# Kernel tuning notes

Hardware: AMD Instinct MI355X
Metric: run time of the kernel (lower is better)

The kernel has to match this reference:

```python
import jax, jax.numpy as jnp
import numpy as np

MARGIN = 1.0
EPS = 1e-16


def _pairwise_dist(x):
    # Euclidean cdist, p=2: sqrt(||a||^2 + ||b||^2 - 2 a.b), clamped, with
    # a safe sqrt so the (zero-distance) diagonal has zero gradient like torch.cdist.
    sq = jnp.sum(x * x, axis=1)  # [N]
    d2 = sq[:, None] + sq[None, :] - 2.0 * (x @ x.T)  # [N, N]
    d2 = jnp.maximum(d2, 0.0)
    return jnp.where(d2 > 0.0, jnp.sqrt(jnp.where(d2 > 0.0, d2, 1.0)), 0.0)


def setup_inputs() -> dict:
    key = jax.random.key(0)
    k1, k2 = jax.random.split(key)
    embeddings = jax.random.normal(k1, (384, 512), dtype=jnp.float32)
    labels = jax.random.randint(k2, (384,), 0, 24, dtype=jnp.int64)
    return {"embeddings": embeddings, "labels": labels}


def reference(embeddings, labels):
    dist = _pairwise_dist(embeddings)  # [N, N]
    pos = (labels[:, None] == labels[None, :]).astype(embeddings.dtype)  # [N, N]
    neg = 1.0 - pos
    positive_dist = dist * pos
    negative_dist = dist * neg
    # triplet_loss[a, p, n] = d(a,p)*pos - d(a,n)*neg + margin
    triplet_loss = jax.nn.relu(positive_dist[:, :, None] - negative_dist[:, None, :] + MARGIN)
    valid = pos[:, :, None] * neg[:, None, :]  # [N, N, N]
    num_valid = jnp.sum(valid) + EPS
    return jnp.sum(triplet_loss * valid) / num_valid
```

## Files before the change

kernel.cpp:

```cpp
#include <hip/hip_runtime.h>


#define NPTS 384
#define DIM  512
#define TS   32
#define BK   64
#define PITCH 68
#define NT1  256
#define NT2  384
#define NW2  (NT2 / 64)

__global__ __launch_bounds__(NT1) void dist_tile(const float* __restrict__ X,
                                                 float* __restrict__ D) {
    __shared__ float As[TS * PITCH];
    __shared__ float Bs[TS * PITCH];
    const int t  = threadIdx.x;
    const int tx = t & 15, ty = t >> 4;
    const int bi = blockIdx.y * TS;
    const int bj = blockIdx.x * TS;

    const float4* X4 = (const float4*)X;
    const int r0 = t >> 4, c4 = t & 15;

    float4 pa0, pa1, pb0, pb1;
    int k4 = 0;
    {
        pa0 = X4[(size_t)(bi + r0)      * (DIM/4) + k4 + c4];
        pa1 = X4[(size_t)(bi + r0 + 16) * (DIM/4) + k4 + c4];
        pb0 = X4[(size_t)(bj + r0)      * (DIM/4) + k4 + c4];
        pb1 = X4[(size_t)(bj + r0 + 16) * (DIM/4) + k4 + c4];
        *(float4*)&As[ r0       * PITCH + c4*4] = pa0;
        *(float4*)&As[(r0 + 16) * PITCH + c4*4] = pa1;
        *(float4*)&Bs[ r0       * PITCH + c4*4] = pb0;
        *(float4*)&Bs[(r0 + 16) * PITCH + c4*4] = pb1;
    }
    __syncthreads();

    float acc00 = 0.f, acc01 = 0.f, acc10 = 0.f, acc11 = 0.f;

    for (int kt = 0; kt < DIM / BK; ++kt) {
        if (kt < DIM / BK - 1) {
            k4 = (kt + 1) * (BK / 4);
            pa0 = X4[(size_t)(bi + r0)      * (DIM/4) + k4 + c4];
            pa1 = X4[(size_t)(bi + r0 + 16) * (DIM/4) + k4 + c4];
            pb0 = X4[(size_t)(bj + r0)      * (DIM/4) + k4 + c4];
            pb1 = X4[(size_t)(bj + r0 + 16) * (DIM/4) + k4 + c4];
        }
#pragma unroll
        for (int kk = 0; kk < BK / 4; ++kk) {
            const float4 a0 = *(const float4*)&As[(2*ty)   * PITCH + kk*4];
            const float4 a1 = *(const float4*)&As[(2*ty+1) * PITCH + kk*4];
            const float4 b0 = *(const float4*)&Bs[(2*tx)   * PITCH + kk*4];
            const float4 b1 = *(const float4*)&Bs[(2*tx+1) * PITCH + kk*4];
            float d;
            d = a0.x - b0.x; acc00 = fmaf(d, d, acc00);
            d = a0.y - b0.y; acc00 = fmaf(d, d, acc00);
            d = a0.z - b0.z; acc00 = fmaf(d, d, acc00);
            d = a0.w - b0.w; acc00 = fmaf(d, d, acc00);
            d = a0.x - b1.x; acc01 = fmaf(d, d, acc01);
            d = a0.y - b1.y; acc01 = fmaf(d, d, acc01);
            d = a0.z - b1.z; acc01 = fmaf(d, d, acc01);
            d = a0.w - b1.w; acc01 = fmaf(d, d, acc01);
            d = a1.x - b0.x; acc10 = fmaf(d, d, acc10);
            d = a1.y - b0.y; acc10 = fmaf(d, d, acc10);
            d = a1.z - b0.z; acc10 = fmaf(d, d, acc10);
            d = a1.w - b0.w; acc10 = fmaf(d, d, acc10);
            d = a1.x - b1.x; acc11 = fmaf(d, d, acc11);
            d = a1.y - b1.y; acc11 = fmaf(d, d, acc11);
            d = a1.z - b1.z; acc11 = fmaf(d, d, acc11);
            d = a1.w - b1.w; acc11 = fmaf(d, d, acc11);
        }
        __syncthreads();
        if (kt < DIM / BK - 1) {
            *(float4*)&As[ r0       * PITCH + c4*4] = pa0;
            *(float4*)&As[(r0 + 16) * PITCH + c4*4] = pa1;
            *(float4*)&Bs[ r0       * PITCH + c4*4] = pb0;
            *(float4*)&Bs[(r0 + 16) * PITCH + c4*4] = pb1;
            __syncthreads();
        }
    }

    const int gi = bi + 2*ty, gj = bj + 2*tx;
    *(float2*)&D[(size_t)gi      * NPTS + gj] = make_float2(sqrtf(acc00), sqrtf(acc01));
    *(float2*)&D[(size_t)(gi+1)  * NPTS + gj] = make_float2(sqrtf(acc10), sqrtf(acc11));
}

__global__ __launch_bounds__(NT2) void pair_reduce(const float* __restrict__ D,
                                                   const int* __restrict__ labels,
                                                   float* __restrict__ out) {
    __shared__ float s_dp[NPTS];
    __shared__ float s_dn[NPTS];
    __shared__ int   s_lab[NPTS] __attribute__((aligned(16)));
    __shared__ int   s_cp[NW2], s_cn[NW2];
    __shared__ float s_red[NW2];
    __shared__ int   s_nv[NW2];

    const int t = threadIdx.x, lane = t & 63, w = t >> 6;
    const int a = blockIdx.x;

    const float dv = D[(size_t)a * NPTS + t];
    s_lab[t] = labels[t];
    const int lab_a = labels[a];
    __syncthreads();

    const bool isp = (s_lab[t] == lab_a);
    const unsigned long long m = __ballot(isp);
    if (lane == 0) { s_cp[w] = __popcll(m); s_cn[w] = 64 - __popcll(m); }
    __syncthreads();

    int basep = 0, basen = 0, np = 0, nn = 0;
#pragma unroll
    for (int i = 0; i < NW2; ++i) {
        if (i < w) { basep += s_cp[i]; basen += s_cn[i]; }
        np += s_cp[i]; nn += s_cn[i];
    }
    const unsigned long long blw = (1ull << lane) - 1ull;
    if (isp) s_dp[basep + __popcll(m  & blw)] = dv;
    else     s_dn[basen + __popcll(~m & blw)] = dv;
    __syncthreads();

    const bool  va  = (t < nn);
    const float dna = va ? s_dn[t] : 0.f;
    float local = 0.f;
    for (int p = 0; p < np; ++p) {
        const float c = s_dp[p] + 1.0f;
        if (va) local += fmaxf(c - dna, 0.f);
    }

    const int myl = s_lab[t];
    int npt = 0;
    const int4* L4 = (const int4*)s_lab;
#pragma unroll 8
    for (int j4 = 0; j4 < NPTS / 4; ++j4) {
        const int4 l = L4[j4];
        npt += (l.x == myl) + (l.y == myl) + (l.z == myl) + (l.w == myl);
    }
    int nvl = npt * (NPTS - npt);

    for (int off = 32; off; off >>= 1) {
        local += __shfl_down(local, off, 64);
        nvl   += __shfl_down(nvl,   off, 64);
    }
    if (lane == 0) { s_red[w] = local; s_nv[w] = nvl; }
    __syncthreads();
    if (t == 0) {
        float bs = 0.f; int nv = 0;
#pragma unroll
        for (int i = 0; i < NW2; ++i) { bs += s_red[i]; nv += s_nv[i]; }
        atomicAdd(out, (float)((double)bs / ((double)nv + 1e-16)));
    }
}

extern "C" void kernel_launch(void* const* d_in, const int* in_sizes, int n_in,
                              void* d_out, int out_size, void* d_ws, size_t ws_size,
                              hipStream_t stream) {
    (void)in_sizes; (void)n_in; (void)out_size; (void)ws_size;
    const float* X      = (const float*)d_in[0];
    const int*   labels = (const int*)d_in[1];

    float* Dmat = (float*)d_ws;

    dist_tile  <<<dim3(NPTS / TS, NPTS / TS), dim3(NT1), 0, stream>>>(X, Dmat);
    pair_reduce<<<dim3(NPTS),                 dim3(NT2), 0, stream>>>(Dmat, labels,
                                                                     (float*)d_out);
}
```

Measured before the change: 79.61 us.

## Split distance kernel along K into four partial sums reduced in pair kernel

The distance kernel's K dimension is split into four slices over blockIdx.z, so the grid grows from 144 to 576 blocks. Each block writes unsquared partial sums to its own slab. The pair-reduction kernel loads the four partials, adds them and takes the square root. This is meant to fill more compute units, since 144 blocks underuse the GPU. In exchange it writes and reads four times the workspace and repeats the prologue load in every block.

```diff
diff --git a/kernel.cpp b/kernel.cpp
--- a/kernel.cpp
+++ b/kernel.cpp
@@ -9,21 +9,24 @@
 #define NT1  256
 #define NT2  384
 #define NW2  (NT2 / 64)
+#define KSPLIT 4
+#define KTPB ((DIM / BK) / KSPLIT)
 
 __global__ __launch_bounds__(NT1) void dist_tile(const float* __restrict__ X,
-                                                 float* __restrict__ D) {
+                                                 float* __restrict__ Dp) {
     __shared__ float As[TS * PITCH];
     __shared__ float Bs[TS * PITCH];
     const int t  = threadIdx.x;
     const int tx = t & 15, ty = t >> 4;
     const int bi = blockIdx.y * TS;
     const int bj = blockIdx.x * TS;
+    const int kt0 = blockIdx.z * KTPB;
 
     const float4* X4 = (const float4*)X;
     const int r0 = t >> 4, c4 = t & 15;
 
     float4 pa0, pa1, pb0, pb1;
-    int k4 = 0;
+    int k4 = kt0 * (BK / 4);
     {
         pa0 = X4[(size_t)(bi + r0)      * (DIM/4) + k4 + c4];
         pa1 = X4[(size_t)(bi + r0 + 16) * (DIM/4) + k4 + c4];
@@ -38,8 +41,8 @@
 
     float acc00 = 0.f, acc01 = 0.f, acc10 = 0.f, acc11 = 0.f;
 
-    for (int kt = 0; kt < DIM / BK; ++kt) {
-        if (kt < DIM / BK - 1) {
+    for (int kt = kt0; kt < kt0 + KTPB; ++kt) {
+        if (kt < kt0 + KTPB - 1) {
             k4 = (kt + 1) * (BK / 4);
             pa0 = X4[(size_t)(bi + r0)      * (DIM/4) + k4 + c4];
             pa1 = X4[(size_t)(bi + r0 + 16) * (DIM/4) + k4 + c4];
@@ -71,7 +74,7 @@
             d = a1.w - b1.w; acc11 = fmaf(d, d, acc11);
         }
         __syncthreads();
-        if (kt < DIM / BK - 1) {
+        if (kt < kt0 + KTPB - 1) {
             *(float4*)&As[ r0       * PITCH + c4*4] = pa0;
             *(float4*)&As[(r0 + 16) * PITCH + c4*4] = pa1;
             *(float4*)&Bs[ r0       * PITCH + c4*4] = pb0;
@@ -80,12 +83,13 @@
         }
     }
 
+    float* Dps = Dp + (size_t)blockIdx.z * NPTS * NPTS;
     const int gi = bi + 2*ty, gj = bj + 2*tx;
-    *(float2*)&D[(size_t)gi      * NPTS + gj] = make_float2(sqrtf(acc00), sqrtf(acc01));
-    *(float2*)&D[(size_t)(gi+1)  * NPTS + gj] = make_float2(sqrtf(acc10), sqrtf(acc11));
+    *(float2*)&Dps[(size_t)gi      * NPTS + gj] = make_float2(acc00, acc01);
+    *(float2*)&Dps[(size_t)(gi+1)  * NPTS + gj] = make_float2(acc10, acc11);
 }
 
-__global__ __launch_bounds__(NT2) void pair_reduce(const float* __restrict__ D,
+__global__ __launch_bounds__(NT2) void pair_reduce(const float* __restrict__ Dp,
                                                    const int* __restrict__ labels,
                                                    float* __restrict__ out) {
     __shared__ float s_dp[NPTS];
@@ -98,9 +102,14 @@
     const int t = threadIdx.x, lane = t & 63, w = t >> 6;
     const int a = blockIdx.x;
 
-    const float dv = D[(size_t)a * NPTS + t];
+    const size_t idx = (size_t)a * NPTS + t;
+    const float p0 = Dp[idx];
+    const float p1 = Dp[idx + (size_t)NPTS * NPTS];
+    const float p2 = Dp[idx + (size_t)2 * NPTS * NPTS];
+    const float p3 = Dp[idx + (size_t)3 * NPTS * NPTS];
     s_lab[t] = labels[t];
     const int lab_a = labels[a];
+    const float dv = sqrtf((p0 + p1) + (p2 + p3));
     __syncthreads();
 
     const bool isp = (s_lab[t] == lab_a);
@@ -158,9 +167,9 @@
     const float* X      = (const float*)d_in[0];
     const int*   labels = (const int*)d_in[1];
 
-    float* Dmat = (float*)d_ws;
+    float* Dp = (float*)d_ws;
 
-    dist_tile  <<<dim3(NPTS / TS, NPTS / TS), dim3(NT1), 0, stream>>>(X, Dmat);
-    pair_reduce<<<dim3(NPTS),                 dim3(NT2), 0, stream>>>(Dmat, labels,
-                                                                     (float*)d_out);
+    dist_tile  <<<dim3(NPTS / TS, NPTS / TS, KSPLIT), dim3(NT1), 0, stream>>>(X, Dp);
+    pair_reduce<<<dim3(NPTS),                         dim3(NT2), 0, stream>>>(Dp, labels,
+                                                                              (float*)d_out);
 }
```

Result: slower. 81.82 us (+2.8%).

## Compute pairwise distances with bf16 MFMA via norm expansion

Applied to the files above, without the earlier changes.

Replaces the scalar difference-squared FMA loop with the ||a||^2+||b||^2-2ab form. The dot products now run on bf16 MFMA 16x16x32 instructions. Each block stages its full 32x512 row panels in shared memory as bf16 with an XOR swizzle, and computes row norms from the same bf16 data. This removes most of the FP32 ALU work and the K-loop synchronisations, but cuts input precision to bf16 and uses 64KB of LDS per block, which may limit occupancy and risk tolerance failures.

```diff
diff --git a/kernel.cpp b/kernel.cpp
--- a/kernel.cpp
+++ b/kernel.cpp
@@ -3,86 +3,92 @@
 
 #define NPTS 384
 #define DIM  512
-#define TS   32
-#define BK   64
-#define PITCH 68
-#define NT1  256
 #define NT2  384
 #define NW2  (NT2 / 64)
 
-__global__ __launch_bounds__(NT1) void dist_tile(const float* __restrict__ X,
+typedef __attribute__((ext_vector_type(8))) short bf16x8;
+typedef __attribute__((ext_vector_type(4))) float f32x4;
+
+__device__ __forceinline__ ushort f2bf(float f) {
+    uint u = __float_as_uint(f);
+    u += 0x7fffu + ((u >> 16) & 1u);
+    return (ushort)(u >> 16);
+}
+
+__global__ __launch_bounds__(256) void dist_mfma(const float* __restrict__ X,
                                                  float* __restrict__ D) {
-    __shared__ float As[TS * PITCH];
-    __shared__ float Bs[TS * PITCH];
-    const int t  = threadIdx.x;
-    const int tx = t & 15, ty = t >> 4;
-    const int bi = blockIdx.y * TS;
-    const int bj = blockIdx.x * TS;
+    __shared__ ushort s_A[32 * 512] __attribute__((aligned(16)));
+    __shared__ ushort s_B[32 * 512] __attribute__((aligned(16)));
+    __shared__ float  s_nrmp[4][64];
+
+    const int t    = threadIdx.x;
+    const int lane = t & 63, w = t >> 6;
+    const int wr   = w >> 1,  wc = w & 1;
+    const int bi   = blockIdx.y * 32;
+    const int bj   = blockIdx.x * 32;
 
     const float4* X4 = (const float4*)X;
-    const int r0 = t >> 4, c4 = t & 15;
 
-    float4 pa0, pa1, pb0, pb1;
-    int k4 = 0;
-    {
-        pa0 = X4[(size_t)(bi + r0)      * (DIM/4) + k4 + c4];
-        pa1 = X4[(size_t)(bi + r0 + 16) * (DIM/4) + k4 + c4];
-        pb0 = X4[(size_t)(bj + r0)      * (DIM/4) + k4 + c4];
-        pb1 = X4[(size_t)(bj + r0 + 16) * (DIM/4) + k4 + c4];
-        *(float4*)&As[ r0       * PITCH + c4*4] = pa0;
-        *(float4*)&As[(r0 + 16) * PITCH + c4*4] = pa1;
-        *(float4*)&Bs[ r0       * PITCH + c4*4] = pb0;
-        *(float4*)&Bs[(r0 + 16) * PITCH + c4*4] = pb1;
+#pragma unroll 8
+    for (int p = 0; p < 32; ++p) {
+        const int idx  = p * 256 + t;
+        const int side = idx >> 12;
+        const int row  = (idx >> 7) & 31;
+        const int col4 = idx & 127;
+        const int grow = (side ? bj : bi) + row;
+        const float4 v = X4[(size_t)grow * 128 + col4];
+        const uint lo = (uint)f2bf(v.x) | ((uint)f2bf(v.y) << 16);
+        const uint hi = (uint)f2bf(v.z) | ((uint)f2bf(v.w) << 16);
+        const int off = (col4 * 8) ^ ((row & 7) << 4);
+        char* dst = (side ? (char*)s_B : (char*)s_A) + row * 1024 + off;
+        *(uint2*)dst = make_uint2(lo, hi);
     }
     __syncthreads();
 
-    float acc00 = 0.f, acc01 = 0.f, acc10 = 0.f, acc11 = 0.f;
-
-    for (int kt = 0; kt < DIM / BK; ++kt) {
-        if (kt < DIM / BK - 1) {
-            k4 = (kt + 1) * (BK / 4);
-            pa0 = X4[(size_t)(bi + r0)      * (DIM/4) + k4 + c4];
-            pa1 = X4[(size_t)(bi + r0 + 16) * (DIM/4) + k4 + c4];
-            pb0 = X4[(size_t)(bj + r0)      * (DIM/4) + k4 + c4];
-            pb1 = X4[(size_t)(bj + r0 + 16) * (DIM/4) + k4 + c4];
+    {
+        const int row  = lane;
+        const int side = row >> 5, r = row & 31;
+        const char* src = (side ? (const char*)s_B : (const char*)s_A) + r * 1024;
+        float nrm = 0.f;
+#pragma unroll
+        for (int c = 0; c < 16; ++c) {
+            const int cb = (w * 16 + c) * 16;
+            const bf16x8 hv = *(const bf16x8*)(src + (cb ^ ((r & 7) << 4)));
+#pragma unroll
+            for (int j = 0; j < 8; ++j) {
+                const float f = __uint_as_float(((uint)(ushort)hv[j]) << 16);
+                nrm = fmaf(f, f, nrm);
+            }
         }
-#pragma unroll
-        for (int kk = 0; kk < BK / 4; ++kk) {
-            const float4 a0 = *(const float4*)&As[(2*ty)   * PITCH + kk*4];
-            const float4 a1 = *(const float4*)&As[(2*ty+1) * PITCH + kk*4];
-            const float4 b0 = *(const float4*)&Bs[(2*tx)   * PITCH + kk*4];
-            const float4 b1 = *(const float4*)&Bs[(2*tx+1) * PITCH + kk*4];
-            float d;
-            d = a0.x - b0.x; acc00 = fmaf(d, d, acc00);
-            d = a0.y - b0.y; acc00 = fmaf(d, d, acc00);
-            d = a0.z - b0.z; acc00 = fmaf(d, d, acc00);
-            d = a0.w - b0.w; acc00 = fmaf(d, d, acc00);
-            d = a0.x - b1.x; acc01 = fmaf(d, d, acc01);
-            d = a0.y - b1.y; acc01 = fmaf(d, d, acc01);
-            d = a0.z - b1.z; acc01 = fmaf(d, d, acc01);
-            d = a0.w - b1.w; acc01 = fmaf(d, d, acc01);
-            d = a1.x - b0.x; acc10 = fmaf(d, d, acc10);
-            d = a1.y - b0.y; acc10 = fmaf(d, d, acc10);
-            d = a1.z - b0.z; acc10 = fmaf(d, d, acc10);
-            d = a1.w - b0.w; acc10 = fmaf(d, d, acc10);
-            d = a1.x - b1.x; acc11 = fmaf(d, d, acc11);
-            d = a1.y - b1.y; acc11 = fmaf(d, d, acc11);
-            d = a1.z - b1.z; acc11 = fmaf(d, d, acc11);
-            d = a1.w - b1.w; acc11 = fmaf(d, d, acc11);
-        }
-        __syncthreads();
-        if (kt < DIM / BK - 1) {
-            *(float4*)&As[ r0       * PITCH + c4*4] = pa0;
-            *(float4*)&As[(r0 + 16) * PITCH + c4*4] = pa1;
-            *(float4*)&Bs[ r0       * PITCH + c4*4] = pb0;
-            *(float4*)&Bs[(r0 + 16) * PITCH + c4*4] = pb1;
-            __syncthreads();
-        }
+        s_nrmp[w][row] = nrm;
     }
 
-    const int gi = bi + 2*ty, gj = bj + 2*tx;
-    *(float2*)&D[(size_t)gi      * NPTS + gj] = make_float2(sqrtf(acc00), sqrtf(acc01));
-    *(float2*)&D[(size_t)(gi+1)  * NPTS + gj] = make_float2(sqrtf(acc10), sqrtf(acc11));
+    f32x4 acc = {0.f, 0.f, 0.f, 0.f};
+    const int ar = wr * 16 + (lane & 15);
+    const int br = wc * 16 + (lane & 15);
+    const char* pa = (const char*)s_A + ar * 1024;
+    const char* pb = (const char*)s_B + br * 1024;
+    const int kg = (lane >> 4) * 16;
+#pragma unroll
+    for (int kt = 0; kt < 16; ++kt) {
+        const int kb = kt * 64 + kg;
+        const bf16x8 af = *(const bf16x8*)(pa + (kb ^ ((ar & 7) << 4)));
+        const bf16x8 bf = *(const bf16x8*)(pb + (kb ^ ((br & 7) << 4)));
+        acc = __builtin_amdgcn_mfma_f32_16x16x32_bf16(af, bf, acc, 0, 0, 0);
+    }
+    __syncthreads();
+
+    const float nB = s_nrmp[0][32 + br] + s_nrmp[1][32 + br] +
+                     s_nrmp[2][32 + br] + s_nrmp[3][32 + br];
+#pragma unroll
+    for (int v = 0; v < 4; ++v) {
+        const int il = wr * 16 + (lane >> 4) * 4 + v;
+        const float nA = s_nrmp[0][il] + s_nrmp[1][il] +
+                         s_nrmp[2][il] + s_nrmp[3][il];
+        const float d2 = nA + nB - 2.f * acc[v];
+        const int gi = bi + il, gj = bj + br;
+        D[(size_t)gi * NPTS + gj] = (gi == gj) ? 0.f : sqrtf(fmaxf(d2, 0.f));
+    }
 }
 
 __global__ __launch_bounds__(NT2) void pair_reduce(const float* __restrict__ D,
@@ -160,7 +166,7 @@
 
     float* Dmat = (float*)d_ws;
 
-    dist_tile  <<<dim3(NPTS / TS, NPTS / TS), dim3(NT1), 0, stream>>>(X, Dmat);
+    dist_mfma  <<<dim3(NPTS / 32, NPTS / 32), dim3(256), 0, stream>>>(X, Dmat);
     pair_reduce<<<dim3(NPTS),                 dim3(NT2), 0, stream>>>(Dmat, labels,
                                                                      (float*)d_out);
 }
```

After: 70.80 us. -11.1%, faster.
